# Kernel tuning notes

Measured on AMD Instinct MI355X. Metric: run time of the kernel, lower is better.

The kernel has to match this reference:

```python
import jax, jax.numpy as jnp
import numpy as np

N = 100000   # nodes
E = 1600000  # edges
D = 128      # input feature dim
H = 64       # hidden dim
G = 64       # graphs in batch


def setup_inputs() -> dict:
    key = jax.random.key(0)
    ks = jax.random.split(key, 12)
    x = jax.random.normal(ks[0], (N, D), dtype=jnp.float32)
    ei = jax.random.randint(ks[1], (2, E), 0, N, dtype=jnp.int32)
    ew = jax.random.uniform(ks[2], (E,), dtype=jnp.float32)
    b = jnp.sort(jax.random.randint(ks[3], (N,), 0, G, dtype=jnp.int32))
    s = 0.05
    W1 = jax.random.normal(ks[4], (D, H), jnp.float32) * s
    b1 = jnp.zeros((H,), jnp.float32)
    W2 = jax.random.normal(ks[5], (H, H), jnp.float32) * s
    b2 = jnp.zeros((H,), jnp.float32)
    Wm1 = jax.random.normal(ks[6], (H, 32), jnp.float32) * s
    bm1 = jnp.zeros((32,), jnp.float32)
    Wm2 = jax.random.normal(ks[7], (32, 1), jnp.float32) * s
    bm2 = jnp.zeros((1,), jnp.float32)
    return {"x": x, "ei": ei, "ew": ew, "b": b,
            "W1": W1, "b1": b1, "W2": W2, "b2": b2,
            "Wm1": Wm1, "bm1": bm1, "Wm2": Wm2, "bm2": bm2}


def _gcn_norm(ei, ew, n):
    # PyG gcn_norm with add_self_loops=True (self-loop weight 1)
    loops = jnp.arange(n, dtype=ei.dtype)
    row = jnp.concatenate([ei[0], loops])
    col = jnp.concatenate([ei[1], loops])
    w = jnp.concatenate([ew, jnp.ones((n,), ew.dtype)])
    deg = jax.ops.segment_sum(w, col, num_segments=n)
    dinv = jnp.where(deg > 0, jax.lax.rsqrt(deg), 0.0)
    norm = dinv[row] * w * dinv[col]  # [E+N]
    return row, col, norm


def _gcn_conv(x, W, bias, row, col, norm, n):
    h = x @ W                                   # [N,H] small GEMM
    msg = h[row] * norm[:, None]                # gather over edges
    return jax.ops.segment_sum(msg, col, num_segments=n) + bias


def reference(x, ei, ew, b, W1, b1, W2, b2, Wm1, bm1, Wm2, bm2):
    n = x.shape[0]
    row, col, norm = _gcn_norm(ei, ew, n)
    h = jax.nn.relu(_gcn_conv(x, W1, b1, row, col, norm, n))
    h = jax.nn.relu(_gcn_conv(h, W2, b2, row, col, norm, n))
    # global_mean_pool over batch vector b
    sums = jax.ops.segment_sum(h, b, num_segments=G)
    cnt = jax.ops.segment_sum(jnp.ones((n,), h.dtype), b, num_segments=G)
    pooled = sums / jnp.maximum(cnt, 1.0)[:, None]  # [G,H]
    # MLP head: Linear(H,32) -> ReLU -> Linear(32,1)
    return jax.nn.relu(pooled @ Wm1 + bm1) @ Wm2 + bm2
```

## Files before the change

### kernel.cpp

```cpp
#include <hip/hip_runtime.h>
#include <hip/hip_bf16.h>
#include <hip/hip_fp16.h>


#define DIMH 64
#define BSH 7
#define BSZ 128
#define NBUCK_MAX 1024
#define EPB 4096
#define ESTRIDE 3072
#define CSTRIDE 4096

typedef _Float16 v8h __attribute__((ext_vector_type(8)));
typedef _Float16 v4h __attribute__((ext_vector_type(4)));
typedef _Float16 hv2 __attribute__((ext_vector_type(2)));
typedef float v4f __attribute__((ext_vector_type(4)));

__global__ __launch_bounds__(512) void k_part(const int* __restrict__ row,
                                              const int* __restrict__ col,
                                              const float* __restrict__ ew,
                                              int* __restrict__ cursor,
                                              unsigned long long* __restrict__ part,
                                              int E, int nbuck) {
    __shared__ int h[NBUCK_MAX];
    __shared__ int h2[NBUCK_MAX];
    __shared__ int st[NBUCK_MAX];
    for (int i = threadIdx.x; i < nbuck; i += 512) { h[i] = 0; h2[i] = 0; }
    __syncthreads();
    int ebeg = blockIdx.x * EPB;
    int eend = min(ebeg + EPB, E);
    for (int e = ebeg + threadIdx.x; e < eend; e += 512)
        atomicAdd(&h[col[e] >> BSH], 1);
    __syncthreads();
    for (int i = threadIdx.x; i < nbuck; i += 512) {
        int c = h[i];
        st[i] = c ? i * ESTRIDE + atomicAdd(&cursor[i], c) : 0;
    }
    __syncthreads();
    for (int e = ebeg + threadIdx.x; e < eend; e += 512) {
        int c = col[e];
        int b = c >> BSH;
        int r = atomicAdd(&h2[b], 1);
        int slot = st[b] + r;
        if (slot < (b + 1) * ESTRIDE) {
            unsigned long long rec =
                ((unsigned long long)__float_as_uint(ew[e]) << 32) |
                ((unsigned long long)(unsigned)row[e] << 8) |
                (unsigned)(c & (BSZ - 1));
            part[slot] = rec;
        }
    }
}

__global__ __launch_bounds__(256) void k_sortB(const unsigned long long* __restrict__ part,
                                               const int* __restrict__ cursor,
                                               int2* __restrict__ csr,
                                               unsigned* __restrict__ rp,
                                               float* __restrict__ dinv, int N) {
    __shared__ int cnt[BSZ];
    __shared__ int scn[BSZ];
    __shared__ int cur[BSZ];
    __shared__ float dg[BSZ];
    int b = blockIdx.x;
    int nb0 = b << BSH;
    int nn = min(BSZ, N - nb0);
    int tid = threadIdx.x;
    if (tid < BSZ) { cnt[tid] = 0; dg[tid] = 1.0f; }
    __syncthreads();
    int ebeg = b * ESTRIDE;
    int eend = ebeg + min(cursor[b], ESTRIDE);
    for (int e = ebeg + tid; e < eend; e += 256)
        atomicAdd(&cnt[(int)(part[e] & (BSZ - 1))], 1);
    __syncthreads();
    int pc = 0;
    if (tid < BSZ) pc = min((cnt[tid] + 15) & ~15, 496);
    if (tid < BSZ) scn[tid] = pc;
    __syncthreads();
    for (int o = 1; o < BSZ; o <<= 1) {
        int t = 0;
        if (tid >= o && tid < BSZ) t = scn[tid - o];
        __syncthreads();
        if (tid >= o && tid < BSZ) scn[tid] += t;
        __syncthreads();
    }
    int Pb = b * CSTRIDE;
    int pofs = 0;
    if (tid < BSZ) {
        pofs = scn[tid] - pc;
        cur[tid] = pofs;
        if (tid < nn)
            rp[nb0 + tid] = ((unsigned)(pc >> 4) << 26) | (unsigned)(Pb + pofs);
    }
    __syncthreads();
    for (int e = ebeg + tid; e < eend; e += 256) {
        unsigned long long rec = part[e];
        int cl = (int)(rec & (BSZ - 1));
        float w = __uint_as_float((unsigned)(rec >> 32));
        int slot = atomicAdd(&cur[cl], 1);
        csr[Pb + slot] = make_int2((int)((rec >> 8) & 0xFFFFFF), __float_as_int(w));
        atomicAdd(&dg[cl], w);
    }
    __syncthreads();
    if (tid < nn) {
        int c = min(cnt[tid], pc);
        for (int k = c; k < pc; k++)
            csr[Pb + pofs + k] = make_int2(nb0 + tid, 0);
        dinv[nb0 + tid] = rsqrtf(dg[tid]);
    }
}

__global__ __launch_bounds__(256) void k_gemm_mfma(const float* __restrict__ X,
                                                   const float* __restrict__ W,
                                                   const float* __restrict__ dinv,
                                                   __half* __restrict__ Y, int n) {
    __shared__ _Float16 Wh[128 * 64];
    int tid = threadIdx.x;
    for (int i = tid * 4; i < 128 * 64; i += 256 * 4) {
        float4 w = *(const float4*)&W[i];
        Wh[i]     = (_Float16)w.x;
        Wh[i + 1] = (_Float16)w.y;
        Wh[i + 2] = (_Float16)w.z;
        Wh[i + 3] = (_Float16)w.w;
    }
    __syncthreads();

    int wv = tid >> 6;
    int lane = tid & 63;
    int m = lane & 15;
    int quad = lane >> 4;
    int tile = blockIdx.x * 4 + wv;
    int ntiles = (n + 15) >> 4;
    if (tile >= ntiles) return;

    v8h bf[4][4];
#pragma unroll
    for (int nt = 0; nt < 4; nt++)
#pragma unroll
        for (int s = 0; s < 4; s++)
#pragma unroll
            for (int j = 0; j < 8; j++)
                bf[nt][s][j] = Wh[(s * 32 + quad * 8 + j) * 64 + nt * 16 + m];

    v4f acc[4];
#pragma unroll
    for (int nt = 0; nt < 4; nt++) acc[nt] = (v4f){0.f, 0.f, 0.f, 0.f};

    int row = min(tile * 16 + m, n - 1);
    const float* xr = X + (size_t)row * 128;
#pragma unroll
    for (int s = 0; s < 4; s++) {
        float4 lo = *(const float4*)&xr[s * 32 + quad * 8];
        float4 hi = *(const float4*)&xr[s * 32 + quad * 8 + 4];
        v8h af;
        af[0] = (_Float16)lo.x; af[1] = (_Float16)lo.y;
        af[2] = (_Float16)lo.z; af[3] = (_Float16)lo.w;
        af[4] = (_Float16)hi.x; af[5] = (_Float16)hi.y;
        af[6] = (_Float16)hi.z; af[7] = (_Float16)hi.w;
#pragma unroll
        for (int nt = 0; nt < 4; nt++)
            acc[nt] = __builtin_amdgcn_mfma_f32_16x16x32_f16(af, bf[nt][s], acc[nt], 0, 0, 0);
    }

#pragma unroll
    for (int r = 0; r < 4; r++) {
        int node = tile * 16 + quad * 4 + r;
        if (node < n) {
            float di = dinv[node];
#pragma unroll
            for (int nt = 0; nt < 4; nt++)
                Y[(size_t)node * DIMH + nt * 16 + m] = __float2half(di * acc[nt][r]);
        }
    }
}

__global__ __launch_bounds__(256, 8) void k_agg1f(const __half* __restrict__ Hin,
                                                  const unsigned* __restrict__ rp,
                                                  const int2* __restrict__ csr,
                                                  const float* __restrict__ dinv,
                                                  const float* __restrict__ bias,
                                                  const float* __restrict__ W2,
                                                  __half* __restrict__ T2, int n) {
    __shared__ __align__(16) _Float16 W2T[64 * 68];
    __shared__ __align__(16) _Float16 hbuf[4][DIMH];
    int tid = threadIdx.x;
    for (int idx = tid; idx < 64 * 64; idx += 256) {
        int k = idx >> 6;
        int o = idx & 63;
        W2T[o * 68 + k] = (_Float16)W2[idx];
    }
    __syncthreads();

    int lane = tid & 63;
    int wv = tid >> 6;
    int q = lane >> 4;
    int fp = lane & 15;

    const char* Hb = (const char*)Hin;
    const char* Cb = (const char*)csr;
    int ngroups = (n + 3) >> 2;
    for (int grp = blockIdx.x; grp < ngroups; grp += gridDim.x) {
        int node = grp * 4 + wv;
        if (node >= n) continue;
        unsigned pk = rp[node];
        unsigned pb = ((pk & 0x3FFFFFFu) << 3) + (unsigned)(q << 4);
        int iters = (int)(pk >> 26);
        float a0 = 0.f, a1 = 0.f, a2 = 0.f, a3 = 0.f;
        if (q == 0) {
            uint2 su = *(const uint2*)(Hb + (((unsigned)node << 7) + (unsigned)(fp << 3)));
            float2 f0 = __half22float2(*(__half2*)&su.x);
            float2 f1 = __half22float2(*(__half2*)&su.y);
            a0 = f0.x; a1 = f0.y; a2 = f1.x; a3 = f1.y;
        }
        unsigned fo = (unsigned)(fp << 3);
        int it = 0;
        for (; it + 2 <= iters; it += 2, pb += 256) {
            int4 mA0 = *(const int4*)(Cb + pb);
            int4 mB0 = *(const int4*)(Cb + pb + 64);
            int4 mA1 = *(const int4*)(Cb + pb + 128);
            int4 mB1 = *(const int4*)(Cb + pb + 192);
            uint2 u0 = *(const uint2*)(Hb + (((unsigned)mA0.x << 7) + fo));
            uint2 u1 = *(const uint2*)(Hb + (((unsigned)mA0.z << 7) + fo));
            uint2 u2 = *(const uint2*)(Hb + (((unsigned)mB0.x << 7) + fo));
            uint2 u3 = *(const uint2*)(Hb + (((unsigned)mB0.z << 7) + fo));
            uint2 u4 = *(const uint2*)(Hb + (((unsigned)mA1.x << 7) + fo));
            uint2 u5 = *(const uint2*)(Hb + (((unsigned)mA1.z << 7) + fo));
            uint2 u6 = *(const uint2*)(Hb + (((unsigned)mB1.x << 7) + fo));
            uint2 u7 = *(const uint2*)(Hb + (((unsigned)mB1.z << 7) + fo));
            float w0 = __int_as_float(mA0.y), w1 = __int_as_float(mA0.w);
            float w2 = __int_as_float(mB0.y), w3 = __int_as_float(mB0.w);
            float w4 = __int_as_float(mA1.y), w5 = __int_as_float(mA1.w);
            float w6 = __int_as_float(mB1.y), w7 = __int_as_float(mB1.w);
            float2 f;
            f = __half22float2(*(__half2*)&u0.x); a0 += w0 * f.x; a1 += w0 * f.y;
            f = __half22float2(*(__half2*)&u0.y); a2 += w0 * f.x; a3 += w0 * f.y;
            f = __half22float2(*(__half2*)&u1.x); a0 += w1 * f.x; a1 += w1 * f.y;
            f = __half22float2(*(__half2*)&u1.y); a2 += w1 * f.x; a3 += w1 * f.y;
            f = __half22float2(*(__half2*)&u2.x); a0 += w2 * f.x; a1 += w2 * f.y;
            f = __half22float2(*(__half2*)&u2.y); a2 += w2 * f.x; a3 += w2 * f.y;
            f = __half22float2(*(__half2*)&u3.x); a0 += w3 * f.x; a1 += w3 * f.y;
            f = __half22float2(*(__half2*)&u3.y); a2 += w3 * f.x; a3 += w3 * f.y;
            f = __half22float2(*(__half2*)&u4.x); a0 += w4 * f.x; a1 += w4 * f.y;
            f = __half22float2(*(__half2*)&u4.y); a2 += w4 * f.x; a3 += w4 * f.y;
            f = __half22float2(*(__half2*)&u5.x); a0 += w5 * f.x; a1 += w5 * f.y;
            f = __half22float2(*(__half2*)&u5.y); a2 += w5 * f.x; a3 += w5 * f.y;
            f = __half22float2(*(__half2*)&u6.x); a0 += w6 * f.x; a1 += w6 * f.y;
            f = __half22float2(*(__half2*)&u6.y); a2 += w6 * f.x; a3 += w6 * f.y;
            f = __half22float2(*(__half2*)&u7.x); a0 += w7 * f.x; a1 += w7 * f.y;
            f = __half22float2(*(__half2*)&u7.y); a2 += w7 * f.x; a3 += w7 * f.y;
        }
        if (it < iters) {
            int4 mA = *(const int4*)(Cb + pb);
            int4 mB = *(const int4*)(Cb + pb + 64);
            uint2 u0 = *(const uint2*)(Hb + (((unsigned)mA.x << 7) + fo));
            uint2 u1 = *(const uint2*)(Hb + (((unsigned)mA.z << 7) + fo));
            uint2 u2 = *(const uint2*)(Hb + (((unsigned)mB.x << 7) + fo));
            uint2 u3 = *(const uint2*)(Hb + (((unsigned)mB.z << 7) + fo));
            float w0 = __int_as_float(mA.y), w1 = __int_as_float(mA.w);
            float w2 = __int_as_float(mB.y), w3 = __int_as_float(mB.w);
            float2 f;
            f = __half22float2(*(__half2*)&u0.x); a0 += w0 * f.x; a1 += w0 * f.y;
            f = __half22float2(*(__half2*)&u0.y); a2 += w0 * f.x; a3 += w0 * f.y;
            f = __half22float2(*(__half2*)&u1.x); a0 += w1 * f.x; a1 += w1 * f.y;
            f = __half22float2(*(__half2*)&u1.y); a2 += w1 * f.x; a3 += w1 * f.y;
            f = __half22float2(*(__half2*)&u2.x); a0 += w2 * f.x; a1 += w2 * f.y;
            f = __half22float2(*(__half2*)&u2.y); a2 += w2 * f.x; a3 += w2 * f.y;
            f = __half22float2(*(__half2*)&u3.x); a0 += w3 * f.x; a1 += w3 * f.y;
            f = __half22float2(*(__half2*)&u3.y); a2 += w3 * f.x; a3 += w3 * f.y;
        }
        a0 += __shfl_xor(a0, 16, 64); a0 += __shfl_xor(a0, 32, 64);
        a1 += __shfl_xor(a1, 16, 64); a1 += __shfl_xor(a1, 32, 64);
        a2 += __shfl_xor(a2, 16, 64); a2 += __shfl_xor(a2, 32, 64);
        a3 += __shfl_xor(a3, 16, 64); a3 += __shfl_xor(a3, 32, 64);
        float di = dinv[node];
        if (q == 0) {
            float4 bs = *(const float4*)&bias[fp * 4];
            float v0 = fmaxf(di * a0 + bs.x, 0.f);
            float v1 = fmaxf(di * a1 + bs.y, 0.f);
            float v2 = fmaxf(di * a2 + bs.z, 0.f);
            float v3 = fmaxf(di * a3 + bs.w, 0.f);
            __half2 h0 = __floats2half2_rn(v0, v1);
            __half2 h1 = __floats2half2_rn(v2, v3);
            uint2 o;
            o.x = *(unsigned*)&h0;
            o.y = *(unsigned*)&h1;
            *(uint2*)&hbuf[wv][fp * 4] = o;
        }
        float accA = 0.f, accB = 0.f;
#pragma unroll
        for (int k8 = 0; k8 < 8; k8++) {
            v8h hv = *(const v8h*)&hbuf[wv][k8 * 8];
            v4h wa = *(const v4h*)&W2T[lane * 68 + k8 * 8];
            v4h wb = *(const v4h*)&W2T[lane * 68 + k8 * 8 + 4];
            hv2 h0 = {hv[0], hv[1]}, h1 = {hv[2], hv[3]};
            hv2 h2_ = {hv[4], hv[5]}, h3 = {hv[6], hv[7]};
            hv2 w0 = {wa[0], wa[1]}, w1 = {wa[2], wa[3]};
            hv2 w2_ = {wb[0], wb[1]}, w3 = {wb[2], wb[3]};
            accA = __builtin_amdgcn_fdot2(h0, w0, accA, false);
            accB = __builtin_amdgcn_fdot2(h1, w1, accB, false);
            accA = __builtin_amdgcn_fdot2(h2_, w2_, accA, false);
            accB = __builtin_amdgcn_fdot2(h3, w3, accB, false);
        }
        T2[(size_t)node * DIMH + lane] = __float2half(di * (accA + accB));
    }
}

__global__ __launch_bounds__(256, 8) void k_aggN(const __half* __restrict__ Hin,
                                                 const unsigned* __restrict__ rp,
                                                 const int2* __restrict__ csr,
                                                 const float* __restrict__ dinv,
                                                 const float* __restrict__ bias,
                                                 __half* __restrict__ Hout, int n) {
    int lane = threadIdx.x & 63;
    int wv = threadIdx.x >> 6;
    int node = blockIdx.x * 4 + wv;
    if (node >= n) return;
    unsigned pk = rp[node];
    int iters = (int)(pk >> 26);
    int q = lane >> 4;
    int fp = lane & 15;
    unsigned pb = ((pk & 0x3FFFFFFu) << 3) + (unsigned)(q << 4);
    unsigned fo = (unsigned)(fp << 3);
    const char* Hb = (const char*)Hin;
    const char* Cb = (const char*)csr;
    float a0 = 0.f, a1 = 0.f, a2 = 0.f, a3 = 0.f;
    if (q == 0) {
        uint2 su = *(const uint2*)(Hb + (((unsigned)node << 7) + fo));
        float2 f0 = __half22float2(*(__half2*)&su.x);
        float2 f1 = __half22float2(*(__half2*)&su.y);
        a0 = f0.x; a1 = f0.y; a2 = f1.x; a3 = f1.y;
    }
    int it = 0;
    for (; it + 2 <= iters; it += 2, pb += 256) {
        int4 mA0 = *(const int4*)(Cb + pb);
        int4 mB0 = *(const int4*)(Cb + pb + 64);
        int4 mA1 = *(const int4*)(Cb + pb + 128);
        int4 mB1 = *(const int4*)(Cb + pb + 192);
        uint2 u0 = *(const uint2*)(Hb + (((unsigned)mA0.x << 7) + fo));
        uint2 u1 = *(const uint2*)(Hb + (((unsigned)mA0.z << 7) + fo));
        uint2 u2 = *(const uint2*)(Hb + (((unsigned)mB0.x << 7) + fo));
        uint2 u3 = *(const uint2*)(Hb + (((unsigned)mB0.z << 7) + fo));
        uint2 u4 = *(const uint2*)(Hb + (((unsigned)mA1.x << 7) + fo));
        uint2 u5 = *(const uint2*)(Hb + (((unsigned)mA1.z << 7) + fo));
        uint2 u6 = *(const uint2*)(Hb + (((unsigned)mB1.x << 7) + fo));
        uint2 u7 = *(const uint2*)(Hb + (((unsigned)mB1.z << 7) + fo));
        float w0 = __int_as_float(mA0.y), w1 = __int_as_float(mA0.w);
        float w2 = __int_as_float(mB0.y), w3 = __int_as_float(mB0.w);
        float w4 = __int_as_float(mA1.y), w5 = __int_as_float(mA1.w);
        float w6 = __int_as_float(mB1.y), w7 = __int_as_float(mB1.w);
        float2 f;
        f = __half22float2(*(__half2*)&u0.x); a0 += w0 * f.x; a1 += w0 * f.y;
        f = __half22float2(*(__half2*)&u0.y); a2 += w0 * f.x; a3 += w0 * f.y;
        f = __half22float2(*(__half2*)&u1.x); a0 += w1 * f.x; a1 += w1 * f.y;
        f = __half22float2(*(__half2*)&u1.y); a2 += w1 * f.x; a3 += w1 * f.y;
        f = __half22float2(*(__half2*)&u2.x); a0 += w2 * f.x; a1 += w2 * f.y;
        f = __half22float2(*(__half2*)&u2.y); a2 += w2 * f.x; a3 += w2 * f.y;
        f = __half22float2(*(__half2*)&u3.x); a0 += w3 * f.x; a1 += w3 * f.y;
        f = __half22float2(*(__half2*)&u3.y); a2 += w3 * f.x; a3 += w3 * f.y;
        f = __half22float2(*(__half2*)&u4.x); a0 += w4 * f.x; a1 += w4 * f.y;
        f = __half22float2(*(__half2*)&u4.y); a2 += w4 * f.x; a3 += w4 * f.y;
        f = __half22float2(*(__half2*)&u5.x); a0 += w5 * f.x; a1 += w5 * f.y;
        f = __half22float2(*(__half2*)&u5.y); a2 += w5 * f.x; a3 += w5 * f.y;
        f = __half22float2(*(__half2*)&u6.x); a0 += w6 * f.x; a1 += w6 * f.y;
        f = __half22float2(*(__half2*)&u6.y); a2 += w6 * f.x; a3 += w6 * f.y;
        f = __half22float2(*(__half2*)&u7.x); a0 += w7 * f.x; a1 += w7 * f.y;
        f = __half22float2(*(__half2*)&u7.y); a2 += w7 * f.x; a3 += w7 * f.y;
    }
    if (it < iters) {
        int4 mA = *(const int4*)(Cb + pb);
        int4 mB = *(const int4*)(Cb + pb + 64);
        uint2 u0 = *(const uint2*)(Hb + (((unsigned)mA.x << 7) + fo));
        uint2 u1 = *(const uint2*)(Hb + (((unsigned)mA.z << 7) + fo));
        uint2 u2 = *(const uint2*)(Hb + (((unsigned)mB.x << 7) + fo));
        uint2 u3 = *(const uint2*)(Hb + (((unsigned)mB.z << 7) + fo));
        float w0 = __int_as_float(mA.y), w1 = __int_as_float(mA.w);
        float w2 = __int_as_float(mB.y), w3 = __int_as_float(mB.w);
        float2 f;
        f = __half22float2(*(__half2*)&u0.x); a0 += w0 * f.x; a1 += w0 * f.y;
        f = __half22float2(*(__half2*)&u0.y); a2 += w0 * f.x; a3 += w0 * f.y;
        f = __half22float2(*(__half2*)&u1.x); a0 += w1 * f.x; a1 += w1 * f.y;
        f = __half22float2(*(__half2*)&u1.y); a2 += w1 * f.x; a3 += w1 * f.y;
        f = __half22float2(*(__half2*)&u2.x); a0 += w2 * f.x; a1 += w2 * f.y;
        f = __half22float2(*(__half2*)&u2.y); a2 += w2 * f.x; a3 += w2 * f.y;
        f = __half22float2(*(__half2*)&u3.x); a0 += w3 * f.x; a1 += w3 * f.y;
        f = __half22float2(*(__half2*)&u3.y); a2 += w3 * f.x; a3 += w3 * f.y;
    }
    a0 += __shfl_xor(a0, 16, 64); a0 += __shfl_xor(a0, 32, 64);
    a1 += __shfl_xor(a1, 16, 64); a1 += __shfl_xor(a1, 32, 64);
    a2 += __shfl_xor(a2, 16, 64); a2 += __shfl_xor(a2, 32, 64);
    a3 += __shfl_xor(a3, 16, 64); a3 += __shfl_xor(a3, 32, 64);
    if (q == 0) {
        float di = dinv[node];
        float4 bs = *(const float4*)&bias[fp * 4];
        float v0 = fmaxf(di * a0 + bs.x, 0.f);
        float v1 = fmaxf(di * a1 + bs.y, 0.f);
        float v2 = fmaxf(di * a2 + bs.z, 0.f);
        float v3 = fmaxf(di * a3 + bs.w, 0.f);
        __half2 h0 = __floats2half2_rn(v0, v1);
        __half2 h1 = __floats2half2_rn(v2, v3);
        uint2 o;
        o.x = *(unsigned*)&h0;
        o.y = *(unsigned*)&h1;
        *(uint2*)&Hout[(size_t)node * DIMH + fp * 4] = o;
    }
}

__global__ __launch_bounds__(256) void k_pool(const __half* __restrict__ Hin,
                                              const int* __restrict__ b,
                                              float* __restrict__ sums,
                                              float* __restrict__ cntG, int n) {
    const int CHUNK = 64;
    int lane = threadIdx.x & 63;
    int wave = threadIdx.x >> 6;
    int start = (blockIdx.x * 4 + wave) * CHUNK;
    if (start >= n) return;
    int end = min(start + CHUNK, n);
    float acc = 0.f;
    int g_cur = b[start];
    int cnt_local = 0;
    for (int i = start; i < end; i++) {
        int g = b[i];
        if (g != g_cur) {
            atomicAdd(&sums[g_cur * DIMH + lane], acc);
            if (lane == 0) atomicAdd(&cntG[g_cur], (float)cnt_local);
            acc = 0.f;
            cnt_local = 0;
            g_cur = g;
        }
        acc += __half2float(Hin[(size_t)i * DIMH + lane]);
        cnt_local++;
    }
    atomicAdd(&sums[g_cur * DIMH + lane], acc);
    if (lane == 0) atomicAdd(&cntG[g_cur], (float)cnt_local);
}

__global__ __launch_bounds__(64) void k_mlp(const float* __restrict__ sums,
                                            const float* __restrict__ cntG,
                                            const float* __restrict__ Wm1,
                                            const float* __restrict__ bm1,
                                            const float* __restrict__ Wm2,
                                            const float* __restrict__ bm2,
                                            float* __restrict__ out, int G) {
    int g = threadIdx.x;
    if (g >= G) return;
    float c = cntG[g];
    float inv = 1.f / (c > 1.f ? c : 1.f);
    float pooled[DIMH];
#pragma unroll
    for (int k = 0; k < DIMH; k++) pooled[k] = sums[g * DIMH + k] * inv;
    float o = 0.f;
    for (int j = 0; j < 32; j++) {
        float t = bm1[j];
#pragma unroll
        for (int k = 0; k < DIMH; k++) t += pooled[k] * Wm1[k * 32 + j];
        t = t > 0.f ? t : 0.f;
        o += t * Wm2[j];
    }
    out[g] = o + bm2[0];
}


extern "C" void kernel_launch(void* const* d_in, const int* in_sizes, int n_in,
                              void* d_out, int out_size, void* d_ws, size_t ws_size,
                              hipStream_t stream) {
    const float* x   = (const float*)d_in[0];
    const int*   ei  = (const int*)d_in[1];
    const float* ew  = (const float*)d_in[2];
    const int*   bvec= (const int*)d_in[3];
    const float* W1  = (const float*)d_in[4];
    const float* b1  = (const float*)d_in[5];
    const float* W2  = (const float*)d_in[6];
    const float* b2  = (const float*)d_in[7];
    const float* Wm1 = (const float*)d_in[8];
    const float* bm1 = (const float*)d_in[9];
    const float* Wm2 = (const float*)d_in[10];
    const float* bm2 = (const float*)d_in[11];
    float* out = (float*)d_out;

    const int E = in_sizes[2];
    const int N = in_sizes[3];
    const int G = out_size;
    const int* row = ei;
    const int* col = ei + E;
    const int nbuck = (N + BSZ - 1) >> BSH;

    char* p = (char*)d_ws;
    auto alloc = [&](size_t bytes) {
        void* r = (void*)p;
        p += (bytes + 255) & ~(size_t)255;
        return r;
    };

    unsigned long long* part = (unsigned long long*)alloc((size_t)nbuck * ESTRIDE * 8);
    int2*  csr    = (int2*)alloc((size_t)nbuck * CSTRIDE * 8);
    unsigned* rp  = (unsigned*)alloc((size_t)N * 4);
    float* dinv   = (float*)alloc((size_t)N * 4);
    __half* hA    = (__half*)alloc((size_t)N * DIMH * 2);
    __half* hB    = (__half*)alloc((size_t)N * DIMH * 2);
    int zeroInts  = nbuck + G * DIMH + G;
    int* cursor   = (int*)alloc((size_t)zeroInts * 4);
    float* sums   = (float*)(cursor + nbuck);
    float* cntG   = sums + G * DIMH;

    hipMemsetAsync(cursor, 0, (size_t)zeroInts * 4, stream);

    const int PB = (E + EPB - 1) / EPB;
    const int NT = (N + 15) / 16;

    k_part<<<PB, 512, 0, stream>>>(row, col, ew, cursor, part, E, nbuck);
    k_sortB<<<nbuck, 256, 0, stream>>>(part, cursor, csr, rp, dinv, N);

    k_gemm_mfma<<<(NT + 3) / 4, 256, 0, stream>>>(x, W1, dinv, hA, N);

    k_agg1f<<<4096, 256, 0, stream>>>(hA, rp, csr, dinv, b1, W2, hB, N);

    k_aggN<<<(N + 3) / 4, 256, 0, stream>>>(hB, rp, csr, dinv, b2, hA, N);

    k_pool<<<(N + 255) / 256, 256, 0, stream>>>(hA, bvec, sums, cntG, N);
    k_mlp<<<1, 64, 0, stream>>>(sums, cntG, Wm1, bm1, Wm2, bm2, out, G);
}
```

Measured before the change: 312.6 us.

## Fuse second aggregation with mean pooling, cut CSR padding to 8, cache cols

The second GCN aggregation now writes its outputs straight into the per-graph pooled sums. Each block reduces its four nodes through shared memory and issues double-precision atomics, so the hidden output is never written to memory and the separate pool kernel is dropped. CSR row padding falls from 16 to 8 edges, with the aggregation loops handling 4-, 2- and 1-group tails to save wasted gathers on padded slots. k_part also keeps column indices in registers so col is read only once. The cost is more contention on global atomics across about 25k blocks, and double-precision atomics are slower.

```diff
diff --git a/kernel.cpp b/kernel.cpp
--- a/kernel.cpp
+++ b/kernel.cpp
@@ -29,16 +29,22 @@
     __syncthreads();
     int ebeg = blockIdx.x * EPB;
     int eend = min(ebeg + EPB, E);
-    for (int e = ebeg + threadIdx.x; e < eend; e += 512)
-        atomicAdd(&h[col[e] >> BSH], 1);
+    int myc[8];
+    int m = 0;
+    for (int e = ebeg + threadIdx.x; e < eend; e += 512) {
+        int c = col[e];
+        myc[m++] = c;
+        atomicAdd(&h[c >> BSH], 1);
+    }
     __syncthreads();
     for (int i = threadIdx.x; i < nbuck; i += 512) {
         int c = h[i];
         st[i] = c ? i * ESTRIDE + atomicAdd(&cursor[i], c) : 0;
     }
     __syncthreads();
-    for (int e = ebeg + threadIdx.x; e < eend; e += 512) {
-        int c = col[e];
+    m = 0;
+    for (int e = ebeg + threadIdx.x; e < eend; e += 512, m++) {
+        int c = myc[m];
         int b = c >> BSH;
         int r = atomicAdd(&h2[b], 1);
         int slot = st[b] + r;
@@ -73,7 +79,7 @@
         atomicAdd(&cnt[(int)(part[e] & (BSZ - 1))], 1);
     __syncthreads();
     int pc = 0;
-    if (tid < BSZ) pc = min((cnt[tid] + 15) & ~15, 496);
+    if (tid < BSZ) pc = min((cnt[tid] + 7) & ~7, 496);
     if (tid < BSZ) scn[tid] = pc;
     __syncthreads();
     for (int o = 1; o < BSZ; o <<= 1) {
@@ -89,7 +95,7 @@
         pofs = scn[tid] - pc;
         cur[tid] = pofs;
         if (tid < nn)
-            rp[nb0 + tid] = ((unsigned)(pc >> 4) << 26) | (unsigned)(Pb + pofs);
+            rp[nb0 + tid] = ((unsigned)(pc >> 3) << 26) | (unsigned)(Pb + pofs);
     }
     __syncthreads();
     for (int e = ebeg + tid; e < eend; e += 256) {
@@ -203,7 +209,7 @@
         if (node >= n) continue;
         unsigned pk = rp[node];
         unsigned pb = ((pk & 0x3FFFFFFu) << 3) + (unsigned)(q << 4);
-        int iters = (int)(pk >> 26);
+        int g8 = (int)(pk >> 26);
         float a0 = 0.f, a1 = 0.f, a2 = 0.f, a3 = 0.f;
         if (q == 0) {
             uint2 su = *(const uint2*)(Hb + (((unsigned)node << 7) + (unsigned)(fp << 3)));
@@ -213,7 +219,7 @@
         }
         unsigned fo = (unsigned)(fp << 3);
         int it = 0;
-        for (; it + 2 <= iters; it += 2, pb += 256) {
+        for (; it + 4 <= g8; it += 4, pb += 256) {
             int4 mA0 = *(const int4*)(Cb + pb);
             int4 mB0 = *(const int4*)(Cb + pb + 64);
             int4 mA1 = *(const int4*)(Cb + pb + 128);
@@ -248,7 +254,7 @@
             f = __half22float2(*(__half2*)&u7.x); a0 += w7 * f.x; a1 += w7 * f.y;
             f = __half22float2(*(__half2*)&u7.y); a2 += w7 * f.x; a3 += w7 * f.y;
         }
-        if (it < iters) {
+        if (it + 2 <= g8) {
             int4 mA = *(const int4*)(Cb + pb);
             int4 mB = *(const int4*)(Cb + pb + 64);
             uint2 u0 = *(const uint2*)(Hb + (((unsigned)mA.x << 7) + fo));
@@ -266,6 +272,18 @@
             f = __half22float2(*(__half2*)&u2.y); a2 += w2 * f.x; a3 += w2 * f.y;
             f = __half22float2(*(__half2*)&u3.x); a0 += w3 * f.x; a1 += w3 * f.y;
             f = __half22float2(*(__half2*)&u3.y); a2 += w3 * f.x; a3 += w3 * f.y;
+            pb += 128; it += 2;
+        }
+        if (it < g8) {
+            int4 mA = *(const int4*)(Cb + pb);
+            uint2 u0 = *(const uint2*)(Hb + (((unsigned)mA.x << 7) + fo));
+            uint2 u1 = *(const uint2*)(Hb + (((unsigned)mA.z << 7) + fo));
+            float w0 = __int_as_float(mA.y), w1 = __int_as_float(mA.w);
+            float2 f;
+            f = __half22float2(*(__half2*)&u0.x); a0 += w0 * f.x; a1 += w0 * f.y;
+            f = __half22float2(*(__half2*)&u0.y); a2 += w0 * f.x; a3 += w0 * f.y;
+            f = __half22float2(*(__half2*)&u1.x); a0 += w1 * f.x; a1 += w1 * f.y;
+            f = __half22float2(*(__half2*)&u1.y); a2 += w1 * f.x; a3 += w1 * f.y;
         }
         a0 += __shfl_xor(a0, 16, 64); a0 += __shfl_xor(a0, 32, 64);
         a1 += __shfl_xor(a1, 16, 64); a1 += __shfl_xor(a1, 32, 64);
@@ -304,137 +322,162 @@
     }
 }
 
-__global__ __launch_bounds__(256, 8) void k_aggN(const __half* __restrict__ Hin,
-                                                 const unsigned* __restrict__ rp,
-                                                 const int2* __restrict__ csr,
-                                                 const float* __restrict__ dinv,
-                                                 const float* __restrict__ bias,
-                                                 __half* __restrict__ Hout, int n) {
-    int lane = threadIdx.x & 63;
-    int wv = threadIdx.x >> 6;
+__global__ __launch_bounds__(256, 8) void k_aggNp(const __half* __restrict__ Hin,
+                                                  const unsigned* __restrict__ rp,
+                                                  const int2* __restrict__ csr,
+                                                  const float* __restrict__ dinv,
+                                                  const float* __restrict__ bias,
+                                                  const int* __restrict__ bvec,
+                                                  double* __restrict__ sums,
+                                                  double* __restrict__ cntG, int n) {
+    __shared__ float wavebuf[4][64];
+    __shared__ int gbuf[4];
+    int tid = threadIdx.x;
+    int lane = tid & 63;
+    int wv = tid >> 6;
     int node = blockIdx.x * 4 + wv;
-    if (node >= n) return;
-    unsigned pk = rp[node];
-    int iters = (int)(pk >> 26);
+    bool valid = node < n;
     int q = lane >> 4;
     int fp = lane & 15;
-    unsigned pb = ((pk & 0x3FFFFFFu) << 3) + (unsigned)(q << 4);
-    unsigned fo = (unsigned)(fp << 3);
-    const char* Hb = (const char*)Hin;
-    const char* Cb = (const char*)csr;
     float a0 = 0.f, a1 = 0.f, a2 = 0.f, a3 = 0.f;
+    if (valid) {
+        unsigned pk = rp[node];
+        int g8 = (int)(pk >> 26);
+        unsigned pb = ((pk & 0x3FFFFFFu) << 3) + (unsigned)(q << 4);
+        unsigned fo = (unsigned)(fp << 3);
+        const char* Hb = (const char*)Hin;
+        const char* Cb = (const char*)csr;
+        if (q == 0) {
+            uint2 su = *(const uint2*)(Hb + (((unsigned)node << 7) + fo));
+            float2 f0 = __half22float2(*(__half2*)&su.x);
+            float2 f1 = __half22float2(*(__half2*)&su.y);
+            a0 = f0.x; a1 = f0.y; a2 = f1.x; a3 = f1.y;
+        }
+        int it = 0;
+        for (; it + 4 <= g8; it += 4, pb += 256) {
+            int4 mA0 = *(const int4*)(Cb + pb);
+            int4 mB0 = *(const int4*)(Cb + pb + 64);
+            int4 mA1 = *(const int4*)(Cb + pb + 128);
+            int4 mB1 = *(const int4*)(Cb + pb + 192);
+            uint2 u0 = *(const uint2*)(Hb + (((unsigned)mA0.x << 7) + fo));
+            uint2 u1 = *(const uint2*)(Hb + (((unsigned)mA0.z << 7) + fo));
+            uint2 u2 = *(const uint2*)(Hb + (((unsigned)mB0.x << 7) + fo));
+            uint2 u3 = *(const uint2*)(Hb + (((unsigned)mB0.z << 7) + fo));
+            uint2 u4 = *(const uint2*)(Hb + (((unsigned)mA1.x << 7) + fo));
+            uint2 u5 = *(const uint2*)(Hb + (((unsigned)mA1.z << 7) + fo));
+            uint2 u6 = *(const uint2*)(Hb + (((unsigned)mB1.x << 7) + fo));
+            uint2 u7 = *(const uint2*)(Hb + (((unsigned)mB1.z << 7) + fo));
+            float w0 = __int_as_float(mA0.y), w1 = __int_as_float(mA0.w);
+            float w2 = __int_as_float(mB0.y), w3 = __int_as_float(mB0.w);
+            float w4 = __int_as_float(mA1.y), w5 = __int_as_float(mA1.w);
+            float w6 = __int_as_float(mB1.y), w7 = __int_as_float(mB1.w);
+            float2 f;
+            f = __half22float2(*(__half2*)&u0.x); a0 += w0 * f.x; a1 += w0 * f.y;
+            f = __half22float2(*(__half2*)&u0.y); a2 += w0 * f.x; a3 += w0 * f.y;
+            f = __half22float2(*(__half2*)&u1.x); a0 += w1 * f.x; a1 += w1 * f.y;
+            f = __half22float2(*(__half2*)&u1.y); a2 += w1 * f.x; a3 += w1 * f.y;
+            f = __half22float2(*(__half2*)&u2.x); a0 += w2 * f.x; a1 += w2 * f.y;
+            f = __half22float2(*(__half2*)&u2.y); a2 += w2 * f.x; a3 += w2 * f.y;
+            f = __half22float2(*(__half2*)&u3.x); a0 += w3 * f.x; a1 += w3 * f.y;
+            f = __half22float2(*(__half2*)&u3.y); a2 += w3 * f.x; a3 += w3 * f.y;
+            f = __half22float2(*(__half2*)&u4.x); a0 += w4 * f.x; a1 += w4 * f.y;
+            f = __half22float2(*(__half2*)&u4.y); a2 += w4 * f.x; a3 += w4 * f.y;
+            f = __half22float2(*(__half2*)&u5.x); a0 += w5 * f.x; a1 += w5 * f.y;
+            f = __half22float2(*(__half2*)&u5.y); a2 += w5 * f.x; a3 += w5 * f.y;
+            f = __half22float2(*(__half2*)&u6.x); a0 += w6 * f.x; a1 += w6 * f.y;
+            f = __half22float2(*(__half2*)&u6.y); a2 += w6 * f.x; a3 += w6 * f.y;
+            f = __half22float2(*(__half2*)&u7.x); a0 += w7 * f.x; a1 += w7 * f.y;
+            f = __half22float2(*(__half2*)&u7.y); a2 += w7 * f.x; a3 += w7 * f.y;
+        }
+        if (it + 2 <= g8) {
+            int4 mA = *(const int4*)(Cb + pb);
+            int4 mB = *(const int4*)(Cb + pb + 64);
+            uint2 u0 = *(const uint2*)(Hb + (((unsigned)mA.x << 7) + fo));
+            uint2 u1 = *(const uint2*)(Hb + (((unsigned)mA.z << 7) + fo));
+            uint2 u2 = *(const uint2*)(Hb + (((unsigned)mB.x << 7) + fo));
+            uint2 u3 = *(const uint2*)(Hb + (((unsigned)mB.z << 7) + fo));
+            float w0 = __int_as_float(mA.y), w1 = __int_as_float(mA.w);
+            float w2 = __int_as_float(mB.y), w3 = __int_as_float(mB.w);
+            float2 f;
+            f = __half22float2(*(__half2*)&u0.x); a0 += w0 * f.x; a1 += w0 * f.y;
+            f = __half22float2(*(__half2*)&u0.y); a2 += w0 * f.x; a3 += w0 * f.y;
+            f = __half22float2(*(__half2*)&u1.x); a0 += w1 * f.x; a1 += w1 * f.y;
+            f = __half22float2(*(__half2*)&u1.y); a2 += w1 * f.x; a3 += w1 * f.y;
+            f = __half22float2(*(__half2*)&u2.x); a0 += w2 * f.x; a1 += w2 * f.y;
+            f = __half22float2(*(__half2*)&u2.y); a2 += w2 * f.x; a3 += w2 * f.y;
+            f = __half22float2(*(__half2*)&u3.x); a0 += w3 * f.x; a1 += w3 * f.y;
+            f = __half22float2(*(__half2*)&u3.y); a2 += w3 * f.x; a3 += w3 * f.y;
+            pb += 128; it += 2;
+        }
+        if (it < g8) {
+            int4 mA = *(const int4*)(Cb + pb);
+            uint2 u0 = *(const uint2*)(Hb + (((unsigned)mA.x << 7) + fo));
+            uint2 u1 = *(const uint2*)(Hb + (((unsigned)mA.z << 7) + fo));
+            float w0 = __int_as_float(mA.y), w1 = __int_as_float(mA.w);
+            float2 f;
+            f = __half22float2(*(__half2*)&u0.x); a0 += w0 * f.x; a1 += w0 * f.y;
+            f = __half22float2(*(__half2*)&u0.y); a2 += w0 * f.x; a3 += w0 * f.y;
+            f = __half22float2(*(__half2*)&u1.x); a0 += w1 * f.x; a1 += w1 * f.y;
+            f = __half22float2(*(__half2*)&u1.y); a2 += w1 * f.x; a3 += w1 * f.y;
+        }
+        a0 += __shfl_xor(a0, 16, 64); a0 += __shfl_xor(a0, 32, 64);
+        a1 += __shfl_xor(a1, 16, 64); a1 += __shfl_xor(a1, 32, 64);
+        a2 += __shfl_xor(a2, 16, 64); a2 += __shfl_xor(a2, 32, 64);
+        a3 += __shfl_xor(a3, 16, 64); a3 += __shfl_xor(a3, 32, 64);
+    }
     if (q == 0) {
-        uint2 su = *(const uint2*)(Hb + (((unsigned)node << 7) + fo));
-        float2 f0 = __half22float2(*(__half2*)&su.x);
-        float2 f1 = __half22float2(*(__half2*)&su.y);
-        a0 = f0.x; a1 = f0.y; a2 = f1.x; a3 = f1.y;
-    }
-    int it = 0;
-    for (; it + 2 <= iters; it += 2, pb += 256) {
-        int4 mA0 = *(const int4*)(Cb + pb);
-        int4 mB0 = *(const int4*)(Cb + pb + 64);
-        int4 mA1 = *(const int4*)(Cb + pb + 128);
-        int4 mB1 = *(const int4*)(Cb + pb + 192);
-        uint2 u0 = *(const uint2*)(Hb + (((unsigned)mA0.x << 7) + fo));
-        uint2 u1 = *(const uint2*)(Hb + (((unsigned)mA0.z << 7) + fo));
-        uint2 u2 = *(const uint2*)(Hb + (((unsigned)mB0.x << 7) + fo));
-        uint2 u3 = *(const uint2*)(Hb + (((unsigned)mB0.z << 7) + fo));
-        uint2 u4 = *(const uint2*)(Hb + (((unsigned)mA1.x << 7) + fo));
-        uint2 u5 = *(const uint2*)(Hb + (((unsigned)mA1.z << 7) + fo));
-        uint2 u6 = *(const uint2*)(Hb + (((unsigned)mB1.x << 7) + fo));
-        uint2 u7 = *(const uint2*)(Hb + (((unsigned)mB1.z << 7) + fo));
-        float w0 = __int_as_float(mA0.y), w1 = __int_as_float(mA0.w);
-        float w2 = __int_as_float(mB0.y), w3 = __int_as_float(mB0.w);
-        float w4 = __int_as_float(mA1.y), w5 = __int_as_float(mA1.w);
-        float w6 = __int_as_float(mB1.y), w7 = __int_as_float(mB1.w);
-        float2 f;
-        f = __half22float2(*(__half2*)&u0.x); a0 += w0 * f.x; a1 += w0 * f.y;
-        f = __half22float2(*(__half2*)&u0.y); a2 += w0 * f.x; a3 += w0 * f.y;
-        f = __half22float2(*(__half2*)&u1.x); a0 += w1 * f.x; a1 += w1 * f.y;
-        f = __half22float2(*(__half2*)&u1.y); a2 += w1 * f.x; a3 += w1 * f.y;
-        f = __half22float2(*(__half2*)&u2.x); a0 += w2 * f.x; a1 += w2 * f.y;
-        f = __half22float2(*(__half2*)&u2.y); a2 += w2 * f.x; a3 += w2 * f.y;
-        f = __half22float2(*(__half2*)&u3.x); a0 += w3 * f.x; a1 += w3 * f.y;
-        f = __half22float2(*(__half2*)&u3.y); a2 += w3 * f.x; a3 += w3 * f.y;
-        f = __half22float2(*(__half2*)&u4.x); a0 += w4 * f.x; a1 += w4 * f.y;
-        f = __half22float2(*(__half2*)&u4.y); a2 += w4 * f.x; a3 += w4 * f.y;
-        f = __half22float2(*(__half2*)&u5.x); a0 += w5 * f.x; a1 += w5 * f.y;
-        f = __half22float2(*(__half2*)&u5.y); a2 += w5 * f.x; a3 += w5 * f.y;
-        f = __half22float2(*(__half2*)&u6.x); a0 += w6 * f.x; a1 += w6 * f.y;
-        f = __half22float2(*(__half2*)&u6.y); a2 += w6 * f.x; a3 += w6 * f.y;
-        f = __half22float2(*(__half2*)&u7.x); a0 += w7 * f.x; a1 += w7 * f.y;
-        f = __half22float2(*(__half2*)&u7.y); a2 += w7 * f.x; a3 += w7 * f.y;
-    }
-    if (it < iters) {
-        int4 mA = *(const int4*)(Cb + pb);
-        int4 mB = *(const int4*)(Cb + pb + 64);
-        uint2 u0 = *(const uint2*)(Hb + (((unsigned)mA.x << 7) + fo));
-        uint2 u1 = *(const uint2*)(Hb + (((unsigned)mA.z << 7) + fo));
-        uint2 u2 = *(const uint2*)(Hb + (((unsigned)mB.x << 7) + fo));
-        uint2 u3 = *(const uint2*)(Hb + (((unsigned)mB.z << 7) + fo));
-        float w0 = __int_as_float(mA.y), w1 = __int_as_float(mA.w);
-        float w2 = __int_as_float(mB.y), w3 = __int_as_float(mB.w);
-        float2 f;
-        f = __half22float2(*(__half2*)&u0.x); a0 += w0 * f.x; a1 += w0 * f.y;
-        f = __half22float2(*(__half2*)&u0.y); a2 += w0 * f.x; a3 += w0 * f.y;
-        f = __half22float2(*(__half2*)&u1.x); a0 += w1 * f.x; a1 += w1 * f.y;
-        f = __half22float2(*(__half2*)&u1.y); a2 += w1 * f.x; a3 += w1 * f.y;
-        f = __half22float2(*(__half2*)&u2.x); a0 += w2 * f.x; a1 += w2 * f.y;
-        f = __half22float2(*(__half2*)&u2.y); a2 += w2 * f.x; a3 += w2 * f.y;
-        f = __half22float2(*(__half2*)&u3.x); a0 += w3 * f.x; a1 += w3 * f.y;
-        f = __half22float2(*(__half2*)&u3.y); a2 += w3 * f.x; a3 += w3 * f.y;
-    }
-    a0 += __shfl_xor(a0, 16, 64); a0 += __shfl_xor(a0, 32, 64);
-    a1 += __shfl_xor(a1, 16, 64); a1 += __shfl_xor(a1, 32, 64);
-    a2 += __shfl_xor(a2, 16, 64); a2 += __shfl_xor(a2, 32, 64);
-    a3 += __shfl_xor(a3, 16, 64); a3 += __shfl_xor(a3, 32, 64);
-    if (q == 0) {
-        float di = dinv[node];
+        float di = valid ? dinv[node] : 0.f;
         float4 bs = *(const float4*)&bias[fp * 4];
-        float v0 = fmaxf(di * a0 + bs.x, 0.f);
-        float v1 = fmaxf(di * a1 + bs.y, 0.f);
-        float v2 = fmaxf(di * a2 + bs.z, 0.f);
-        float v3 = fmaxf(di * a3 + bs.w, 0.f);
-        __half2 h0 = __floats2half2_rn(v0, v1);
-        __half2 h1 = __floats2half2_rn(v2, v3);
-        uint2 o;
-        o.x = *(unsigned*)&h0;
-        o.y = *(unsigned*)&h1;
-        *(uint2*)&Hout[(size_t)node * DIMH + fp * 4] = o;
-    }
-}
-
-__global__ __launch_bounds__(256) void k_pool(const __half* __restrict__ Hin,
-                                              const int* __restrict__ b,
-                                              float* __restrict__ sums,
-                                              float* __restrict__ cntG, int n) {
-    const int CHUNK = 64;
-    int lane = threadIdx.x & 63;
-    int wave = threadIdx.x >> 6;
-    int start = (blockIdx.x * 4 + wave) * CHUNK;
-    if (start >= n) return;
-    int end = min(start + CHUNK, n);
-    float acc = 0.f;
-    int g_cur = b[start];
-    int cnt_local = 0;
-    for (int i = start; i < end; i++) {
-        int g = b[i];
-        if (g != g_cur) {
-            atomicAdd(&sums[g_cur * DIMH + lane], acc);
-            if (lane == 0) atomicAdd(&cntG[g_cur], (float)cnt_local);
-            acc = 0.f;
-            cnt_local = 0;
-            g_cur = g;
-        }
-        acc += __half2float(Hin[(size_t)i * DIMH + lane]);
-        cnt_local++;
-    }
-    atomicAdd(&sums[g_cur * DIMH + lane], acc);
-    if (lane == 0) atomicAdd(&cntG[g_cur], (float)cnt_local);
-}
-
-__global__ __launch_bounds__(64) void k_mlp(const float* __restrict__ sums,
-                                            const float* __restrict__ cntG,
+        float v0 = valid ? fmaxf(di * a0 + bs.x, 0.f) : 0.f;
+        float v1 = valid ? fmaxf(di * a1 + bs.y, 0.f) : 0.f;
+        float v2 = valid ? fmaxf(di * a2 + bs.z, 0.f) : 0.f;
+        float v3 = valid ? fmaxf(di * a3 + bs.w, 0.f) : 0.f;
+        wavebuf[wv][fp * 4 + 0] = v0;
+        wavebuf[wv][fp * 4 + 1] = v1;
+        wavebuf[wv][fp * 4 + 2] = v2;
+        wavebuf[wv][fp * 4 + 3] = v3;
+    }
+    if (lane == 0) gbuf[wv] = valid ? bvec[node] : -1;
+    __syncthreads();
+    if (tid < 64) {
+        int g0 = gbuf[0];
+        float s = 0.f;
+#pragma unroll
+        for (int w = 0; w < 4; w++)
+            if (gbuf[w] == g0) s += wavebuf[w][tid];
+        if (g0 >= 0) atomicAdd(&sums[g0 * 64 + tid], (double)s);
+#pragma unroll
+        for (int w = 1; w < 4; w++) {
+            int gw = gbuf[w];
+            if (gw < 0 || gw == g0) continue;
+            bool dup = false;
+            for (int u = 1; u < w; u++)
+                if (gbuf[u] == gw) dup = true;
+            if (dup) continue;
+            float s2 = 0.f;
+            for (int u = w; u < 4; u++)
+                if (gbuf[u] == gw) s2 += wavebuf[u][tid];
+            atomicAdd(&sums[gw * 64 + tid], (double)s2);
+        }
+    } else if (tid == 64) {
+#pragma unroll
+        for (int w = 0; w < 4; w++) {
+            int gw = gbuf[w];
+            if (gw < 0) continue;
+            bool first = true;
+            for (int u = 0; u < w; u++)
+                if (gbuf[u] == gw) first = false;
+            if (!first) continue;
+            double c = 0.0;
+            for (int u = w; u < 4; u++)
+                if (gbuf[u] == gw) c += 1.0;
+            atomicAdd(&cntG[gw], c);
+        }
+    }
+}
+
+__global__ __launch_bounds__(64) void k_mlp(const double* __restrict__ sums,
+                                            const double* __restrict__ cntG,
                                             const float* __restrict__ Wm1,
                                             const float* __restrict__ bm1,
                                             const float* __restrict__ Wm2,
@@ -442,11 +485,11 @@
                                             float* __restrict__ out, int G) {
     int g = threadIdx.x;
     if (g >= G) return;
-    float c = cntG[g];
+    float c = (float)cntG[g];
     float inv = 1.f / (c > 1.f ? c : 1.f);
     float pooled[DIMH];
 #pragma unroll
-    for (int k = 0; k < DIMH; k++) pooled[k] = sums[g * DIMH + k] * inv;
+    for (int k = 0; k < DIMH; k++) pooled[k] = (float)sums[g * DIMH + k] * inv;
     float o = 0.f;
     for (int j = 0; j < 32; j++) {
         float t = bm1[j];
@@ -496,15 +539,16 @@
     float* dinv   = (float*)alloc((size_t)N * 4);
     __half* hA    = (__half*)alloc((size_t)N * DIMH * 2);
     __half* hB    = (__half*)alloc((size_t)N * DIMH * 2);
-    int zeroInts  = nbuck + G * DIMH + G;
-    int* cursor   = (int*)alloc((size_t)zeroInts * 4);
-    float* sums   = (float*)(cursor + nbuck);
-    float* cntG   = sums + G * DIMH;
-
-    hipMemsetAsync(cursor, 0, (size_t)zeroInts * 4, stream);
+    size_t zeroBytes = (size_t)G * DIMH * 8 + (size_t)G * 8 + (size_t)nbuck * 4;
+    double* sums  = (double*)alloc(zeroBytes);
+    double* cntG  = sums + (size_t)G * DIMH;
+    int* cursor   = (int*)(cntG + G);
+
+    hipMemsetAsync(sums, 0, zeroBytes, stream);
 
     const int PB = (E + EPB - 1) / EPB;
     const int NT = (N + 15) / 16;
+    const int NG = (N + 3) / 4;
 
     k_part<<<PB, 512, 0, stream>>>(row, col, ew, cursor, part, E, nbuck);
     k_sortB<<<nbuck, 256, 0, stream>>>(part, cursor, csr, rp, dinv, N);
@@ -513,8 +557,7 @@
 
     k_agg1f<<<4096, 256, 0, stream>>>(hA, rp, csr, dinv, b1, W2, hB, N);
 
-    k_aggN<<<(N + 3) / 4, 256, 0, stream>>>(hB, rp, csr, dinv, b2, hA, N);
-
-    k_pool<<<(N + 255) / 256, 256, 0, stream>>>(hA, bvec, sums, cntG, N);
+    k_aggNp<<<NG, 256, 0, stream>>>(hB, rp, csr, dinv, b2, bvec, sums, cntG, N);
+
     k_mlp<<<1, 64, 0, stream>>>(sums, cntG, Wm1, bm1, Wm2, bm2, out, G);
 }
```

After: 402.5 us. 1.29x slower.
